# Performance work log

Hardware: AMD Instinct MI355X
Metric: run time of the kernel (lower is better)

Reference implementation:

```python
import jax, jax.numpy as jnp
import numpy as np

N_LAYERS = 4
NEG_SLOPE = 0.2  # GATv2 leaky_relu slope


def _segment_softmax(alpha, seg, num):
    # alpha: [E, H], seg: [E] target-node ids; every node has a self loop so no empty segments
    amax = jax.ops.segment_max(alpha, seg, num_segments=num)
    a = jnp.exp(alpha - amax[seg])
    denom = jax.ops.segment_sum(a, seg, num_segments=num)
    return a / denom[seg]


def _gat_block(x, relations, src, dst, rel_idx, Wl, bl, Wr, br, We, att, bias, Wb, bb):
    N, D = x.shape
    H = att.shape[0]
    C = att.shape[1]

    edge_attr = relations[rel_idx]  # [E, D]
    # add_self_loops with fill_value='mean': self-loop edge_attr = mean of incoming edge attrs
    deg = jax.ops.segment_sum(jnp.ones_like(dst, dtype=x.dtype), dst, num_segments=N)
    loop_attr = jax.ops.segment_sum(edge_attr, dst, num_segments=N) / jnp.maximum(deg, 1.0)[:, None]
    loops = jnp.arange(N, dtype=src.dtype)
    src_all = jnp.concatenate([src, loops])
    dst_all = jnp.concatenate([dst, loops])
    ea = jnp.concatenate([edge_attr, loop_attr], axis=0)  # [E+N, D]

    xl = (x @ Wl + bl).reshape(N, H, C)  # lin_l -> source transform
    xr = (x @ Wr + br).reshape(N, H, C)  # lin_r -> target transform
    eproj = (ea @ We).reshape(-1, H, C)  # lin_edge (no bias in PyG GATv2Conv)

    m = xl[src_all] + xr[dst_all] + eproj          # [E+N, H, C]
    m = jnp.where(m > 0, m, NEG_SLOPE * m)          # leaky_relu
    alpha = jnp.einsum('ehc,hc->eh', m, att)        # [E+N, H]
    alpha = _segment_softmax(alpha, dst_all, N)

    msg = xl[src_all] * alpha[..., None]            # [E+N, H, C]
    out = jax.ops.segment_sum(msg, dst_all, num_segments=N)  # [N, H, C]
    x_out = out.mean(axis=1) + bias                 # concat=False -> head mean, then bias

    # relation update: gnn.lin_edge -> relu -> block lin_edge
    r = jax.nn.relu(relations @ We)                 # [R, H*C]
    r_out = r @ Wb + bb                             # [R, D]
    return x_out, r_out


def setup_inputs() -> dict:
    key = jax.random.key(0)
    N, E, R, D, H = 10000, 40000, 2000, 128, 8
    L = N_LAYERS
    ks = jax.random.split(key, 16)
    s = 1.0 / np.sqrt(D)
    sb = 1.0 / np.sqrt(H * D)
    return {
        'x': jax.random.normal(ks[0], (N, D), dtype=jnp.float32),
        'edge_index': jax.random.randint(ks[1], (2, E), 0, N),
        'relations': jax.random.normal(ks[2], (R, D), dtype=jnp.float32),
        'relation_index': jax.random.randint(ks[3], (E,), 0, R),
        'Wl': jax.random.normal(ks[4], (L, D, H * D), dtype=jnp.float32) * s,
        'bl': jnp.zeros((L, H * D), dtype=jnp.float32),
        'Wr': jax.random.normal(ks[5], (L, D, H * D), dtype=jnp.float32) * s,
        'br': jnp.zeros((L, H * D), dtype=jnp.float32),
        'We': jax.random.normal(ks[6], (L, D, H * D), dtype=jnp.float32) * s,
        'att': jax.random.normal(ks[7], (L, H, D), dtype=jnp.float32) * s,
        'bias': jnp.zeros((L, D), dtype=jnp.float32),
        'Wb': jax.random.normal(ks[8], (L, H * D, D), dtype=jnp.float32) * sb,
        'bb': jnp.zeros((L, D), dtype=jnp.float32),
    }


def reference(x, edge_index, relations, relation_index, Wl, bl, Wr, br, We, att, bias, Wb, bb):
    src, dst = edge_index[0], edge_index[1]
    for l in range(N_LAYERS):
        x, relations = _gat_block(x, relations, src, dst, relation_index,
                                  Wl[l], bl[l], Wr[l], br[l], We[l], att[l],
                                  bias[l], Wb[l], bb[l])
    return (x, relations)
```

## Files before the change

kernel.cpp:

```cpp
#include <hip/hip_runtime.h>
#include <hip/hip_bf16.h>
#include <math.h>

#define NEG_SLOPE 0.2f
#define N_LAYERS 4

typedef __bf16 bf16_t;
typedef __attribute__((ext_vector_type(8))) __bf16 bf16x8;
typedef __attribute__((ext_vector_type(4))) __bf16 bf16x4;
typedef __attribute__((ext_vector_type(4))) float f32x4;
typedef __attribute__((ext_vector_type(8))) float f32x8;

static __device__ __forceinline__ float leaky(float v){ return v > 0.f ? v : NEG_SLOPE * v; }

static __device__ __forceinline__ bf16x8 relu8(bf16x8 v){
#pragma unroll
  for(int i = 0; i < 8; ++i) v[i] = (v[i] > (bf16_t)0.f) ? v[i] : (bf16_t)0.f;
  return v;
}


__global__ void fill_int_kernel(int* __restrict__ p, int v, int n){
  int i = blockIdx.x*blockDim.x + threadIdx.x;
  if(i < n) p[i] = v;
}

__global__ void hist_kernel(const int* __restrict__ dst, int E, int* __restrict__ deg){
  int e = blockIdx.x*blockDim.x + threadIdx.x;
  if(e < E) atomicAdd(&deg[dst[e]], 1);
}

__global__ void scan_kernel(const int* __restrict__ deg, int* __restrict__ offs, int N){
  __shared__ int wsum[4];
  int t = threadIdx.x, lane = t & 63, w = t >> 6;
  int carry = 0;
  for(int base = 0; base < N; base += 256){
    int v = (base + t < N) ? deg[base + t] : 0;
    int s = v;
#pragma unroll
    for(int o = 1; o < 64; o <<= 1){
      int u = __shfl_up(s, o);
      if(lane >= o) s += u;
    }
    if(lane == 63) wsum[w] = s;
    __syncthreads();
    int woff = 0;
    for(int i = 0; i < w; ++i) woff += wsum[i];
    if(base + t < N) offs[base + t + 1] = carry + woff + s;
    int tot = wsum[0] + wsum[1] + wsum[2] + wsum[3];
    __syncthreads();
    carry += tot;
  }
  if(t == 0) offs[0] = 0;
}

__global__ void scatter_kernel(const int* __restrict__ src, const int* __restrict__ dst,
                               const int* __restrict__ rel, int E,
                               const int* __restrict__ offs, int* __restrict__ cursor,
                               int* __restrict__ srcs, int* __restrict__ rels){
  int e = blockIdx.x*blockDim.x + threadIdx.x;
  if(e < E){
    int d = dst[e];
    int pos = offs[d] + atomicAdd(&cursor[d], 1);
    srcs[pos] = src[e];
    rels[pos] = rel[e];
  }
}


__global__ void deg_bhist_kernel(const int* __restrict__ offs, int N, int* __restrict__ blkhist){
  __shared__ int h[256];
  int t = threadIdx.x;
  h[t] = 0; __syncthreads();
  int i = blockIdx.x * 256 + t;
  if(i < N){
    int d = offs[i+1] - offs[i]; if(d > 255) d = 255;
    atomicAdd(&h[d], 1);
  }
  __syncthreads();
  blkhist[blockIdx.x * 256 + t] = h[t];
}

__global__ void deg_base_kernel(int* __restrict__ blkhist, int nb){
  __shared__ int tot[256];
  int d = threadIdx.x;
  int s = 0;
  for(int b = 0; b < nb; ++b){
    int v = blkhist[b * 256 + d];
    blkhist[b * 256 + d] = s;
    s += v;
  }
  tot[d] = s; __syncthreads();
  int start = 0;
  for(int k = d + 1; k < 256; ++k) start += tot[k];
  for(int b = 0; b < nb; ++b) blkhist[b * 256 + d] += start;
}

__global__ void deg_place_kernel(const int* __restrict__ offs, int N,
                                 const int* __restrict__ blkhist, int* __restrict__ order){
  __shared__ int cur[256];
  int t = threadIdx.x;
  cur[t] = blkhist[blockIdx.x * 256 + t];
  __syncthreads();
  int i = blockIdx.x * 256 + t;
  if(i < N){
    int d = offs[i+1] - offs[i]; if(d > 255) d = 255;
    int pos = atomicAdd(&cur[d], 1);
    order[pos] = i;
  }
}


__global__ void transpose_split_all_kernel(
    const float* __restrict__ Wl, const float* __restrict__ Wr,
    const float* __restrict__ We, const float* __restrict__ Wb,
    bf16_t* __restrict__ tWlh, bf16_t* __restrict__ tWll,
    bf16_t* __restrict__ tWrh, bf16_t* __restrict__ tWrl,
    bf16_t* __restrict__ tWeh, bf16_t* __restrict__ tWel,
    bf16_t* __restrict__ tWbh, bf16_t* __restrict__ tWbl){
  __shared__ float t[32][33];
  const int z = blockIdx.z, type = z >> 2, layer = z & 3;
  const int K  = (type < 3) ? 128 : 1024;
  const int Nn = (type < 3) ? 1024 : 128;
  const float* W; bf16_t* Th; bf16_t* Tl;
  if(type == 0){ W = Wl; Th = tWlh; Tl = tWll; }
  else if(type == 1){ W = Wr; Th = tWrh; Tl = tWrl; }
  else if(type == 2){ W = We; Th = tWeh; Tl = tWel; }
  else { W = Wb; Th = tWbh; Tl = tWbl; }
  size_t wo = (size_t)layer * 131072;
  W += wo; Th += wo; Tl += wo;
  const int nbx = K / 32;
  const int bx = blockIdx.x % nbx, by = blockIdx.x / nbx;
  const int k0 = bx * 32, n0 = by * 32;
  const int tx = threadIdx.x, ty = threadIdx.y;
#pragma unroll
  for(int i = 0; i < 4; ++i)
    t[ty*4 + i][tx] = W[(size_t)(k0 + ty*4 + i) * Nn + n0 + tx];
  __syncthreads();
#pragma unroll
  for(int i = 0; i < 4; ++i){
    int n = ty*4 + i;
    float v = t[tx][n];
    bf16_t h = (bf16_t)v;
    bf16_t l = (bf16_t)(v - (float)h);
    Th[(size_t)(n0 + n) * K + k0 + tx] = h;
    Tl[(size_t)(n0 + n) * K + k0 + tx] = l;
  }
}


__global__ __launch_bounds__(256, 3) void gemm_proj_kernel(
    const float* __restrict__ Ar, const float* __restrict__ Ax,
    const bf16_t* __restrict__ Axb,
    const bf16_t* __restrict__ Weh, const bf16_t* __restrict__ Wel,
    const bf16_t* __restrict__ Wlh, const bf16_t* __restrict__ Wll,
    const bf16_t* __restrict__ Wrh, const bf16_t* __restrict__ Wrl,
    const float* __restrict__ biasL, const float* __restrict__ biasR,
    const float* __restrict__ biasB, float* __restrict__ ro,
    bf16_t* __restrict__ rpb, bf16_t* __restrict__ xlb, bf16_t* __restrict__ xrb,
    int R, int Nn, int rjobs, int xjobs, int bjobs){
  constexpr int LDK = 40;
  __shared__ char smem[34816];
  bf16_t* Ah = (bf16_t*)smem;
  bf16_t* Bh = (bf16_t*)(smem + 10240);
  bf16_t* Bl = (bf16_t*)(smem + 20480);

  const int tid  = threadIdx.x;
  const int lane = tid & 63;
  const int wid  = tid >> 6;
  const int wm = wid >> 1, wn = wid & 1;
  const int l15 = lane & 15;
  const int kb  = (lane >> 4) * 8;

  int nwg = gridDim.x;
  int lin = blockIdx.x;
  int w = ((nwg & 7) == 0) ? ((lin & 7) * (nwg >> 3) + (lin >> 3)) : lin;
  int job, jw;
  if(w < rjobs){ job = 0; jw = w; }
  else if(w < rjobs + xjobs){ job = 1; jw = w - rjobs; }
  else if(w < rjobs + 2 * xjobs){ job = 2; jw = w - rjobs - xjobs; }
  else { job = 3; jw = w - rjobs - 2 * xjobs; }

  if(job == 3){
    int idx8 = (jw * 256 + tid) * 8;
    if(idx8 < R * 128){
      const float* bp = biasB + (idx8 & 127);
      *(float4*)(ro + idx8)     = *(const float4*)bp;
      *(float4*)(ro + idx8 + 4) = *(const float4*)(bp + 4);
    }
    return;
  }

  const float*  A   = (job == 0) ? Ar : Ax;
  const bf16_t* Bth = (job == 0) ? Weh : (job == 1) ? Wlh : Wrh;
  const bf16_t* Btl = (job == 0) ? Wel : (job == 1) ? Wll : Wrl;
  const int M = (job == 0) ? R : Nn;
  const int row0 = (jw >> 3) * 128, col0 = (jw & 7) * 128;
  const bool abf = (job != 0) && (Axb != nullptr);

  f32x4 acc[4][4];
#pragma unroll
  for(int m = 0; m < 4; ++m)
#pragma unroll
    for(int n = 0; n < 4; ++n) acc[m][n] = (f32x4){0.f, 0.f, 0.f, 0.f};

  for(int k0 = 0; k0 < 128; k0 += 32){
    __syncthreads();
    if(abf){
#pragma unroll
      for(int i = 0; i < 2; ++i){
        int f = tid + i * 256;
        int r = f >> 2, kq = f & 3;
        bf16x8 v = {};
        if(row0 + r < M) v = *(const bf16x8*)(Axb + (size_t)(row0 + r) * 128 + k0 + kq * 8);
        *(bf16x8*)&Ah[r * LDK + kq * 8] = v;
      }
    } else {
#pragma unroll
      for(int i = 0; i < 4; ++i){
        int f = tid + i * 256;
        int r = f >> 3, kq = f & 7;
        float4 v = make_float4(0.f, 0.f, 0.f, 0.f);
        if(row0 + r < M) v = *(const float4*)(A + (size_t)(row0 + r) * 128 + k0 + kq * 4);
        bf16x4 hv = (bf16x4){(bf16_t)v.x, (bf16_t)v.y, (bf16_t)v.z, (bf16_t)v.w};
        *(bf16x4*)&Ah[r * LDK + kq * 4] = hv;
      }
    }
#pragma unroll
    for(int i = 0; i < 2; ++i){
      int f = tid + i * 256;
      int n = f >> 2, kq = f & 3;
      size_t g = (size_t)(col0 + n) * 128 + k0 + kq * 8;
      *(bf16x8*)&Bh[n * LDK + kq * 8] = *(const bf16x8*)(Bth + g);
      *(bf16x8*)&Bl[n * LDK + kq * 8] = *(const bf16x8*)(Btl + g);
    }
    __syncthreads();

    bf16x8 ah[4], bh[4], bl[4];
#pragma unroll
    for(int m = 0; m < 4; ++m){
      int r = wm * 64 + m * 16 + l15;
      ah[m] = *(bf16x8*)&Ah[r * LDK + kb];
    }
#pragma unroll
    for(int n = 0; n < 4; ++n){
      int c = wn * 64 + n * 16 + l15;
      bh[n] = *(bf16x8*)&Bh[c * LDK + kb];
      bl[n] = *(bf16x8*)&Bl[c * LDK + kb];
    }
#pragma unroll
    for(int m = 0; m < 4; ++m)
#pragma unroll
      for(int n = 0; n < 4; ++n){
        acc[m][n] = __builtin_amdgcn_mfma_f32_16x16x32_bf16(ah[m], bh[n], acc[m][n], 0, 0, 0);
        acc[m][n] = __builtin_amdgcn_mfma_f32_16x16x32_bf16(ah[m], bl[n], acc[m][n], 0, 0, 0);
      }
  }

  const float* biasP = (job == 0) ? nullptr : (job == 1) ? biasL : biasR;
  bf16_t* dst = (job == 0) ? rpb : (job == 1) ? xlb : xrb;
  bf16_t* tile = (bf16_t*)smem;
  __syncthreads();
#pragma unroll
  for(int n = 0; n < 4; ++n){
    int col = wn * 64 + n * 16 + l15;
    float bv = biasP ? biasP[col0 + col] : 0.f;
#pragma unroll
    for(int m = 0; m < 4; ++m){
      int rb = wm * 64 + m * 16 + (lane >> 4) * 4;
#pragma unroll
      for(int r = 0; r < 4; ++r)
        tile[(rb + r) * 136 + col] = (bf16_t)(acc[m][n][r] + bv);
    }
  }
  __syncthreads();
#pragma unroll
  for(int i = 0; i < 8; ++i){
    int ei = i * 2048 + tid * 8;
    int rr = ei >> 7, cc = ei & 127;
    if(row0 + rr < M)
      *(bf16x8*)(dst + (size_t)(row0 + rr) * 1024 + col0 + cc) = *(bf16x8*)&tile[rr * 136 + cc];
  }
}


__global__ __launch_bounds__(256) void gemm_rel_kernel(
    const bf16_t* __restrict__ Ag,
    const bf16_t* __restrict__ Bth, const bf16_t* __restrict__ Btl,
    float* __restrict__ C, int M){
  constexpr int LDK = 40;
  __shared__ bf16_t Ah[128 * LDK];
  __shared__ bf16_t Bh[128 * LDK];
  __shared__ bf16_t Bl[128 * LDK];

  const int tid  = threadIdx.x;
  const int lane = tid & 63;
  const int wid  = tid >> 6;
  const int wm = wid >> 1, wn = wid & 1;
  const int row0 = blockIdx.y * 128;
  const int l15 = lane & 15;
  const int kb  = (lane >> 4) * 8;
  const int kbeg = blockIdx.z * 64;

  f32x4 acc[4][4];
#pragma unroll
  for(int m = 0; m < 4; ++m)
#pragma unroll
    for(int n = 0; n < 4; ++n) acc[m][n] = (f32x4){0.f, 0.f, 0.f, 0.f};

#pragma unroll
  for(int tt = 0; tt < 2; ++tt){
    int k0 = kbeg + tt * 32;
    __syncthreads();
#pragma unroll
    for(int i = 0; i < 2; ++i){
      int f = tid + i * 256;
      int r = f >> 2, kq = f & 3;
      bf16x8 vh = {};
      if(row0 + r < M)
        vh = relu8(*(const bf16x8*)(Ag + (size_t)(row0 + r) * 1024 + k0 + kq * 8));
      *(bf16x8*)&Ah[r * LDK + kq * 8] = vh;
      size_t gb = (size_t)r * 1024 + k0 + kq * 8;
      *(bf16x8*)&Bh[r * LDK + kq * 8] = *(const bf16x8*)(Bth + gb);
      *(bf16x8*)&Bl[r * LDK + kq * 8] = *(const bf16x8*)(Btl + gb);
    }
    __syncthreads();

    bf16x8 ah[4], bh[4], bl[4];
#pragma unroll
    for(int m = 0; m < 4; ++m){
      int r = wm * 64 + m * 16 + l15;
      ah[m] = *(bf16x8*)&Ah[r * LDK + kb];
    }
#pragma unroll
    for(int n = 0; n < 4; ++n){
      int c = wn * 64 + n * 16 + l15;
      bh[n] = *(bf16x8*)&Bh[c * LDK + kb];
      bl[n] = *(bf16x8*)&Bl[c * LDK + kb];
    }
#pragma unroll
    for(int m = 0; m < 4; ++m)
#pragma unroll
      for(int n = 0; n < 4; ++n){
        acc[m][n] = __builtin_amdgcn_mfma_f32_16x16x32_bf16(ah[m], bh[n], acc[m][n], 0, 0, 0);
        acc[m][n] = __builtin_amdgcn_mfma_f32_16x16x32_bf16(ah[m], bl[n], acc[m][n], 0, 0, 0);
      }
  }

#pragma unroll
  for(int n = 0; n < 4; ++n){
    int col = wn * 64 + n * 16 + l15;
    if(col < 128){
#pragma unroll
      for(int m = 0; m < 4; ++m){
        int rbase = row0 + wm * 64 + m * 16 + (lane >> 4) * 4;
#pragma unroll
        for(int r = 0; r < 4; ++r){
          if(rbase + r < M)
            atomicAdd(&C[(size_t)(rbase + r) * 128 + col], acc[m][n][r]);
        }
      }
    }
  }
}


__global__ __launch_bounds__(256) void node_fused_kernel(
    const bf16_t* __restrict__ xlb, const bf16_t* __restrict__ xrb,
    const bf16_t* __restrict__ rpb,
    const int* __restrict__ offs, const int* __restrict__ srcs, const int* __restrict__ rels,
    const int* __restrict__ order,
    const float* __restrict__ att, const float* __restrict__ bias,
    float* __restrict__ xout, bf16_t* __restrict__ xq, int N){
  __shared__ float tsh[2][128];
  const int wid  = threadIdx.x >> 6;
  const int lane = threadIdx.x & 63;
  const int nib  = wid >> 1;
  const int half = wid & 1;
  const int slot = blockIdx.x * 2 + nib;
  const bool active = slot < N;
  const int node = active ? order[slot] : 0;
  int beg = 0, end = 0;
  if(active){ beg = offs[node]; end = offs[node + 1]; }
  const float inv = 1.0f / fmaxf((float)(end - beg), 1.0f);

  const int o  = (half * 64 + lane) * 8;
  const int c0 = (lane & 15) * 8;
  const int h  = half * 4 + (lane >> 4);
  f32x8 av = *(const f32x8*)(att + h * 128 + c0);
  bf16x8 xrv = *(const bf16x8*)(xrb + (size_t)node * 1024 + o);
  f32x8 xr;
#pragma unroll
  for(int i = 0; i < 8; ++i) xr[i] = (float)xrv[i];

  f32x8 lac, num;
#pragma unroll
  for(int i = 0; i < 8; ++i){ lac[i] = 0.f; num[i] = 0.f; }
  float m = -INFINITY, den = 0.f;

  for(int p = beg; p < end; p += 4){
    int rem = end - p;
    int i1 = (rem > 1) ? p + 1 : p;
    int i2 = (rem > 2) ? p + 2 : p;
    int i3 = (rem > 3) ? p + 3 : p;
    float k1 = (rem > 1) ? 1.f : 0.f;
    float k2 = (rem > 2) ? 1.f : 0.f;
    float k3 = (rem > 3) ? 1.f : 0.f;
    int s0 = srcs[p],  r0 = rels[p];
    int s1 = srcs[i1], r1 = rels[i1];
    int s2 = srcs[i2], r2 = rels[i2];
    int s3 = srcs[i3], r3 = rels[i3];
    bf16x8 a0 = *(const bf16x8*)(xlb + (size_t)s0 * 1024 + o);
    bf16x8 b0 = *(const bf16x8*)(rpb + (size_t)r0 * 1024 + o);
    bf16x8 a1 = *(const bf16x8*)(xlb + (size_t)s1 * 1024 + o);
    bf16x8 b1 = *(const bf16x8*)(rpb + (size_t)r1 * 1024 + o);
    bf16x8 a2 = *(const bf16x8*)(xlb + (size_t)s2 * 1024 + o);
    bf16x8 b2 = *(const bf16x8*)(rpb + (size_t)r2 * 1024 + o);
    bf16x8 a3 = *(const bf16x8*)(xlb + (size_t)s3 * 1024 + o);
    bf16x8 b3 = *(const bf16x8*)(rpb + (size_t)r3 * 1024 + o);
    float l0 = 0.f, l1 = 0.f, l2 = 0.f, l3 = 0.f;
#pragma unroll
    for(int i = 0; i < 8; ++i){
      float v0 = (float)b0[i], v1 = (float)b1[i], v2 = (float)b2[i], v3 = (float)b3[i];
      lac[i] += v0 + k1 * v1 + k2 * v2 + k3 * v3;
      l0 += leaky((float)a0[i] + xr[i] + v0) * av[i];
      l1 += leaky((float)a1[i] + xr[i] + v1) * av[i];
      l2 += leaky((float)a2[i] + xr[i] + v2) * av[i];
      l3 += leaky((float)a3[i] + xr[i] + v3) * av[i];
    }
#pragma unroll
    for(int q = 8; q >= 1; q >>= 1){
      l0 += __shfl_xor(l0, q); l1 += __shfl_xor(l1, q);
      l2 += __shfl_xor(l2, q); l3 += __shfl_xor(l3, q);
    }
    l1 = (k1 > 0.f) ? l1 : -INFINITY;
    l2 = (k2 > 0.f) ? l2 : -INFINITY;
    l3 = (k3 > 0.f) ? l3 : -INFINITY;
    float nm = fmaxf(m, fmaxf(fmaxf(l0, l1), fmaxf(l2, l3)));
    float sc = __expf(m - nm);
    float w0 = __expf(l0 - nm), w1 = __expf(l1 - nm);
    float w2 = __expf(l2 - nm), w3 = __expf(l3 - nm);
    den = den * sc + w0 + w1 + w2 + w3;
#pragma unroll
    for(int i = 0; i < 8; ++i)
      num[i] = num[i] * sc + w0 * (float)a0[i] + w1 * (float)a1[i]
                           + w2 * (float)a2[i] + w3 * (float)a3[i];
    m = nm;
  }

  bf16x8 xlv = *(const bf16x8*)(xlb + (size_t)node * 1024 + o);
  float sl = 0.f;
#pragma unroll
  for(int i = 0; i < 8; ++i)
    sl += leaky((float)xlv[i] + xr[i] + lac[i] * inv) * av[i];
#pragma unroll
  for(int q = 8; q >= 1; q >>= 1) sl += __shfl_xor(sl, q);
  {
    float nm = fmaxf(m, sl);
    float sc = __expf(m - nm), wv = __expf(sl - nm);
    den = den * sc + wv;
#pragma unroll
    for(int i = 0; i < 8; ++i) num[i] = num[i] * sc + wv * (float)xlv[i];
    m = nm;
  }

  f32x8 t;
  float d = 1.0f / den;
#pragma unroll
  for(int i = 0; i < 8; ++i) t[i] = num[i] * d;
#pragma unroll
  for(int i = 0; i < 8; ++i) t[i] += __shfl_xor(t[i], 16);
#pragma unroll
  for(int i = 0; i < 8; ++i) t[i] += __shfl_xor(t[i], 32);

  if(half == 1 && lane < 16){
#pragma unroll
    for(int i = 0; i < 8; ++i) tsh[nib][lane * 8 + i] = t[i];
  }
  __syncthreads();
  if(active && half == 0 && lane < 16){
    const float* bp = bias + lane * 8;
    float q[8];
#pragma unroll
    for(int i = 0; i < 8; ++i) q[i] = (t[i] + tsh[nib][lane * 8 + i]) * 0.125f + bp[i];
    bf16x8 qb;
#pragma unroll
    for(int i = 0; i < 8; ++i) qb[i] = (bf16_t)q[i];
    *(bf16x8*)(xq + (size_t)node * 128 + lane * 8) = qb;
    if(xout){
      float* op = xout + (size_t)node * 128 + lane * 8;
      *(float4*)op       = make_float4(q[0], q[1], q[2], q[3]);
      *(float4*)(op + 4) = make_float4(q[4], q[5], q[6], q[7]);
    }
  }
}


extern "C" void kernel_launch(void* const* d_in, const int* in_sizes, int n_in,
                              void* d_out, int out_size, void* d_ws, size_t ws_size,
                              hipStream_t stream){
  const float* x0   = (const float*)d_in[0];
  const int*   ei   = (const int*)d_in[1];
  const float* rel0 = (const float*)d_in[2];
  const int*   ridx = (const int*)d_in[3];
  const float* Wl   = (const float*)d_in[4];
  const float* bl   = (const float*)d_in[5];
  const float* Wr   = (const float*)d_in[6];
  const float* br   = (const float*)d_in[7];
  const float* We   = (const float*)d_in[8];
  const float* att  = (const float*)d_in[9];
  const float* bias = (const float*)d_in[10];
  const float* Wb   = (const float*)d_in[11];
  const float* bb   = (const float*)d_in[12];

  const int D = 128, HC = 1024;
  const int N = in_sizes[0] / D;
  const int E = in_sizes[1] / 2;
  const int R = in_sizes[2] / D;
  const int WSZ = D * HC;
  const int NB = (N + 255) / 256;

  const int* src = ei;
  const int* dst = ei + E;

  char* ws = (char*)d_ws;
  size_t off = 0;
  auto alloc = [&](size_t bytes) -> void* {
    void* p = ws + off;
    off += (bytes + 255) & ~(size_t)255;
    return p;
  };
  bf16_t* xlb    = (bf16_t*)alloc((size_t)N * HC * 2);
  bf16_t* xrb    = (bf16_t*)alloc((size_t)N * HC * 2);
  bf16_t* rpb    = (bf16_t*)alloc((size_t)R * HC * 2);
  bf16_t* xqA    = (bf16_t*)alloc((size_t)N * D * 2);
  bf16_t* xqB    = (bf16_t*)alloc((size_t)N * D * 2);
  float*  rbufA  = (float*)alloc((size_t)R * D * 4);
  float*  rbufB  = (float*)alloc((size_t)R * D * 4);
  int* zbase   = (int*)alloc((size_t)(2 * N) * 4);
  int* deg     = zbase;
  int* cursor  = zbase + N;
  int* offs    = (int*)alloc((size_t)(N + 1) * 4);
  int* blkhist = (int*)alloc((size_t)NB * 256 * 4);
  int* order   = (int*)alloc((size_t)N * 4);
  int* srcs    = (int*)alloc((size_t)E * 4);
  int* rels    = (int*)alloc((size_t)E * 4);
  bf16_t* tWl_h = (bf16_t*)alloc((size_t)N_LAYERS * WSZ * 2);
  bf16_t* tWl_l = (bf16_t*)alloc((size_t)N_LAYERS * WSZ * 2);
  bf16_t* tWr_h = (bf16_t*)alloc((size_t)N_LAYERS * WSZ * 2);
  bf16_t* tWr_l = (bf16_t*)alloc((size_t)N_LAYERS * WSZ * 2);
  bf16_t* tWe_h = (bf16_t*)alloc((size_t)N_LAYERS * WSZ * 2);
  bf16_t* tWe_l = (bf16_t*)alloc((size_t)N_LAYERS * WSZ * 2);
  bf16_t* tWb_h = (bf16_t*)alloc((size_t)N_LAYERS * WSZ * 2);
  bf16_t* tWb_l = (bf16_t*)alloc((size_t)N_LAYERS * WSZ * 2);
  bf16_t* xq[2] = {xqA, xqB};
  float* rbuf[2] = {rbufA, rbufB};

  float* out_x = (float*)d_out;
  float* out_r = (float*)d_out + (size_t)N * D;

  fill_int_kernel<<<(2 * N + 255) / 256, 256, 0, stream>>>(zbase, 0, 2 * N);
  hist_kernel<<<(E + 255) / 256, 256, 0, stream>>>(dst, E, deg);
  scan_kernel<<<1, 256, 0, stream>>>(deg, offs, N);
  scatter_kernel<<<(E + 255) / 256, 256, 0, stream>>>(src, dst, ridx, E, offs, cursor, srcs, rels);
  deg_bhist_kernel<<<NB, 256, 0, stream>>>(offs, N, blkhist);
  deg_base_kernel<<<1, 256, 0, stream>>>(blkhist, NB);
  deg_place_kernel<<<NB, 256, 0, stream>>>(offs, N, blkhist, order);

  transpose_split_all_kernel<<<dim3(128, 1, 16), dim3(32, 8), 0, stream>>>(
      Wl, Wr, We, Wb, tWl_h, tWl_l, tWr_h, tWr_l, tWe_h, tWe_l, tWb_h, tWb_l);

  const int rjobs = ((R + 127) / 128) * (HC / 128);
  const int xjobs = ((N + 127) / 128) * (HC / 128);
  const int bjobs = 128;
  const int nwg = rjobs + 2 * xjobs + bjobs;

  for(int l = 0; l < N_LAYERS; ++l){
    const bf16_t* xq_in = (l == 0) ? nullptr : xq[(l + 1) & 1];
    bf16_t*       xq_out = xq[l & 1];
    float*        xo  = (l == N_LAYERS - 1) ? out_x : nullptr;
    const float*  rin = (l == 0) ? rel0 : rbuf[(l + 1) & 1];
    float*        ro  = (l == N_LAYERS - 1) ? out_r : rbuf[l & 1];
    size_t wo = (size_t)l * WSZ;
    const float* bl_l  = bl + (size_t)l * HC;
    const float* br_l  = br + (size_t)l * HC;
    const float* att_l = att + (size_t)l * 8 * 128;
    const float* bias_l= bias + (size_t)l * D;
    const float* bb_l  = bb + (size_t)l * D;

    gemm_proj_kernel<<<nwg, 256, 0, stream>>>(
        rin, x0, xq_in, tWe_h + wo, tWe_l + wo, tWl_h + wo, tWl_l + wo, tWr_h + wo, tWr_l + wo,
        bl_l, br_l, bb_l, ro, rpb, xlb, xrb, R, N, rjobs, xjobs, bjobs);
    node_fused_kernel<<<(2 * N + 3) / 4, 256, 0, stream>>>(
        xlb, xrb, rpb, offs, srcs, rels, order, att_l, bias_l, xo, xq_out, N);
    gemm_rel_kernel<<<dim3(1, (R + 127) / 128, 16), 256, 0, stream>>>(
        rpb, tWb_h + wo, tWb_l + wo, ro, R);
  }
}
```

Baseline: 395.0 us.

## Merge scatter and degree histogram launches, preload A tile, prefetch edge indices

Three separate changes. The scatter and per-block degree-histogram kernels become one launch whose blocks branch on blockIdx, saving a kernel launch. The projection GEMM now loads the full 128-wide A tile into shared memory once and streams only the B hi/lo slices per k-step, which raises shared memory use and may lower occupancy. The attention aggregation loop software-prefetches the next group of four source/relation indices so the dependent gathers wait less on index loads.

```diff
diff --git a/kernel.cpp b/kernel.cpp
--- a/kernel.cpp
+++ b/kernel.cpp
@@ -54,31 +54,32 @@
   if(t == 0) offs[0] = 0;
 }
 
-__global__ void scatter_kernel(const int* __restrict__ src, const int* __restrict__ dst,
-                               const int* __restrict__ rel, int E,
-                               const int* __restrict__ offs, int* __restrict__ cursor,
-                               int* __restrict__ srcs, int* __restrict__ rels){
-  int e = blockIdx.x*blockDim.x + threadIdx.x;
-  if(e < E){
-    int d = dst[e];
-    int pos = offs[d] + atomicAdd(&cursor[d], 1);
-    srcs[pos] = src[e];
-    rels[pos] = rel[e];
-  }
-}
-
-
-__global__ void deg_bhist_kernel(const int* __restrict__ offs, int N, int* __restrict__ blkhist){
+__global__ void scatter_bhist_kernel(const int* __restrict__ src, const int* __restrict__ dst,
+                                     const int* __restrict__ rel, int E,
+                                     const int* __restrict__ offs, int* __restrict__ cursor,
+                                     int* __restrict__ srcs, int* __restrict__ rels,
+                                     int N, int* __restrict__ blkhist, int SCB){
   __shared__ int h[256];
-  int t = threadIdx.x;
-  h[t] = 0; __syncthreads();
-  int i = blockIdx.x * 256 + t;
-  if(i < N){
-    int d = offs[i+1] - offs[i]; if(d > 255) d = 255;
-    atomicAdd(&h[d], 1);
-  }
-  __syncthreads();
-  blkhist[blockIdx.x * 256 + t] = h[t];
+  if((int)blockIdx.x < SCB){
+    int e = blockIdx.x * 256 + threadIdx.x;
+    if(e < E){
+      int d = dst[e];
+      int pos = offs[d] + atomicAdd(&cursor[d], 1);
+      srcs[pos] = src[e];
+      rels[pos] = rel[e];
+    }
+  } else {
+    int b = blockIdx.x - SCB;
+    int t = threadIdx.x;
+    h[t] = 0; __syncthreads();
+    int i = b * 256 + t;
+    if(i < N){
+      int d = offs[i+1] - offs[i]; if(d > 255) d = 255;
+      atomicAdd(&h[d], 1);
+    }
+    __syncthreads();
+    blkhist[b * 256 + t] = h[t];
+  }
 }
 
 __global__ void deg_base_kernel(int* __restrict__ blkhist, int nb){
@@ -159,11 +160,11 @@
     const float* __restrict__ biasB, float* __restrict__ ro,
     bf16_t* __restrict__ rpb, bf16_t* __restrict__ xlb, bf16_t* __restrict__ xrb,
     int R, int Nn, int rjobs, int xjobs, int bjobs){
-  constexpr int LDK = 40;
-  __shared__ char smem[34816];
-  bf16_t* Ah = (bf16_t*)smem;
-  bf16_t* Bh = (bf16_t*)(smem + 10240);
-  bf16_t* Bl = (bf16_t*)(smem + 20480);
+  constexpr int LDA  = 136;
+  constexpr int LDBB = 72;
+  __shared__ char smem[53248];
+  bf16_t* Ah  = (bf16_t*)smem;
+  bf16_t* Bhl = (bf16_t*)(smem + 34816);
 
   const int tid  = threadIdx.x;
   const int lane = tid & 63;
@@ -198,55 +199,56 @@
   const int row0 = (jw >> 3) * 128, col0 = (jw & 7) * 128;
   const bool abf = (job != 0) && (Axb != nullptr);
 
+  if(abf){
+#pragma unroll
+    for(int i = 0; i < 8; ++i){
+      int f = tid + i * 256;
+      int r = f >> 4, kq = f & 15;
+      bf16x8 v = {};
+      if(row0 + r < M) v = *(const bf16x8*)(Axb + (size_t)(row0 + r) * 128 + kq * 8);
+      *(bf16x8*)&Ah[r * LDA + kq * 8] = v;
+    }
+  } else {
+#pragma unroll
+    for(int i = 0; i < 16; ++i){
+      int f = tid + i * 256;
+      int r = f >> 5, kq = f & 31;
+      float4 v = make_float4(0.f, 0.f, 0.f, 0.f);
+      if(row0 + r < M) v = *(const float4*)(A + (size_t)(row0 + r) * 128 + kq * 4);
+      bf16x4 hv = (bf16x4){(bf16_t)v.x, (bf16_t)v.y, (bf16_t)v.z, (bf16_t)v.w};
+      *(bf16x4*)&Ah[r * LDA + kq * 4] = hv;
+    }
+  }
+#pragma unroll
+  for(int i = 0; i < 2; ++i){
+    int f = tid + i * 256;
+    int n = f >> 2, kq = f & 3;
+    size_t g = (size_t)(col0 + n) * 128 + kq * 8;
+    *(bf16x8*)&Bhl[n * LDBB + kq * 8]      = *(const bf16x8*)(Bth + g);
+    *(bf16x8*)&Bhl[n * LDBB + 32 + kq * 8] = *(const bf16x8*)(Btl + g);
+  }
+  __syncthreads();
+
   f32x4 acc[4][4];
 #pragma unroll
   for(int m = 0; m < 4; ++m)
 #pragma unroll
     for(int n = 0; n < 4; ++n) acc[m][n] = (f32x4){0.f, 0.f, 0.f, 0.f};
 
-  for(int k0 = 0; k0 < 128; k0 += 32){
-    __syncthreads();
-    if(abf){
-#pragma unroll
-      for(int i = 0; i < 2; ++i){
-        int f = tid + i * 256;
-        int r = f >> 2, kq = f & 3;
-        bf16x8 v = {};
-        if(row0 + r < M) v = *(const bf16x8*)(Axb + (size_t)(row0 + r) * 128 + k0 + kq * 8);
-        *(bf16x8*)&Ah[r * LDK + kq * 8] = v;
-      }
-    } else {
-#pragma unroll
-      for(int i = 0; i < 4; ++i){
-        int f = tid + i * 256;
-        int r = f >> 3, kq = f & 7;
-        float4 v = make_float4(0.f, 0.f, 0.f, 0.f);
-        if(row0 + r < M) v = *(const float4*)(A + (size_t)(row0 + r) * 128 + k0 + kq * 4);
-        bf16x4 hv = (bf16x4){(bf16_t)v.x, (bf16_t)v.y, (bf16_t)v.z, (bf16_t)v.w};
-        *(bf16x4*)&Ah[r * LDK + kq * 4] = hv;
-      }
-    }
-#pragma unroll
-    for(int i = 0; i < 2; ++i){
-      int f = tid + i * 256;
-      int n = f >> 2, kq = f & 3;
-      size_t g = (size_t)(col0 + n) * 128 + k0 + kq * 8;
-      *(bf16x8*)&Bh[n * LDK + kq * 8] = *(const bf16x8*)(Bth + g);
-      *(bf16x8*)&Bl[n * LDK + kq * 8] = *(const bf16x8*)(Btl + g);
-    }
-    __syncthreads();
-
+#pragma unroll
+  for(int step = 0; step < 4; ++step){
+    const int k0 = step * 32;
     bf16x8 ah[4], bh[4], bl[4];
 #pragma unroll
     for(int m = 0; m < 4; ++m){
       int r = wm * 64 + m * 16 + l15;
-      ah[m] = *(bf16x8*)&Ah[r * LDK + kb];
+      ah[m] = *(bf16x8*)&Ah[r * LDA + k0 + kb];
     }
 #pragma unroll
     for(int n = 0; n < 4; ++n){
       int c = wn * 64 + n * 16 + l15;
-      bh[n] = *(bf16x8*)&Bh[c * LDK + kb];
-      bl[n] = *(bf16x8*)&Bl[c * LDK + kb];
+      bh[n] = *(bf16x8*)&Bhl[c * LDBB + kb];
+      bl[n] = *(bf16x8*)&Bhl[c * LDBB + 32 + kb];
     }
 #pragma unroll
     for(int m = 0; m < 4; ++m)
@@ -255,11 +257,23 @@
         acc[m][n] = __builtin_amdgcn_mfma_f32_16x16x32_bf16(ah[m], bh[n], acc[m][n], 0, 0, 0);
         acc[m][n] = __builtin_amdgcn_mfma_f32_16x16x32_bf16(ah[m], bl[n], acc[m][n], 0, 0, 0);
       }
+    if(step < 3){
+      __syncthreads();
+#pragma unroll
+      for(int i = 0; i < 2; ++i){
+        int f = tid + i * 256;
+        int n = f >> 2, kq = f & 3;
+        size_t g = (size_t)(col0 + n) * 128 + k0 + 32 + kq * 8;
+        *(bf16x8*)&Bhl[n * LDBB + kq * 8]      = *(const bf16x8*)(Bth + g);
+        *(bf16x8*)&Bhl[n * LDBB + 32 + kq * 8] = *(const bf16x8*)(Btl + g);
+      }
+      __syncthreads();
+    }
   }
 
   const float* biasP = (job == 0) ? nullptr : (job == 1) ? biasL : biasR;
   bf16_t* dst = (job == 0) ? rpb : (job == 1) ? xlb : xrb;
-  bf16_t* tile = (bf16_t*)smem;
+  bf16_t* tile = Ah;
   __syncthreads();
 #pragma unroll
   for(int n = 0; n < 4; ++n){
@@ -398,26 +412,50 @@
   for(int i = 0; i < 8; ++i){ lac[i] = 0.f; num[i] = 0.f; }
   float m = -INFINITY, den = 0.f;
 
-  for(int p = beg; p < end; p += 4){
+  int p = beg;
+  int cs0 = 0, cs1 = 0, cs2 = 0, cs3 = 0, cr0 = 0, cr1 = 0, cr2 = 0, cr3 = 0;
+  float k1 = 0.f, k2 = 0.f, k3 = 0.f;
+  if(p < end){
     int rem = end - p;
     int i1 = (rem > 1) ? p + 1 : p;
     int i2 = (rem > 2) ? p + 2 : p;
     int i3 = (rem > 3) ? p + 3 : p;
-    float k1 = (rem > 1) ? 1.f : 0.f;
-    float k2 = (rem > 2) ? 1.f : 0.f;
-    float k3 = (rem > 3) ? 1.f : 0.f;
-    int s0 = srcs[p],  r0 = rels[p];
-    int s1 = srcs[i1], r1 = rels[i1];
-    int s2 = srcs[i2], r2 = rels[i2];
-    int s3 = srcs[i3], r3 = rels[i3];
-    bf16x8 a0 = *(const bf16x8*)(xlb + (size_t)s0 * 1024 + o);
-    bf16x8 b0 = *(const bf16x8*)(rpb + (size_t)r0 * 1024 + o);
-    bf16x8 a1 = *(const bf16x8*)(xlb + (size_t)s1 * 1024 + o);
-    bf16x8 b1 = *(const bf16x8*)(rpb + (size_t)r1 * 1024 + o);
-    bf16x8 a2 = *(const bf16x8*)(xlb + (size_t)s2 * 1024 + o);
-    bf16x8 b2 = *(const bf16x8*)(rpb + (size_t)r2 * 1024 + o);
-    bf16x8 a3 = *(const bf16x8*)(xlb + (size_t)s3 * 1024 + o);
-    bf16x8 b3 = *(const bf16x8*)(rpb + (size_t)r3 * 1024 + o);
+    k1 = (rem > 1) ? 1.f : 0.f;
+    k2 = (rem > 2) ? 1.f : 0.f;
+    k3 = (rem > 3) ? 1.f : 0.f;
+    cs0 = srcs[p];  cr0 = rels[p];
+    cs1 = srcs[i1]; cr1 = rels[i1];
+    cs2 = srcs[i2]; cr2 = rels[i2];
+    cs3 = srcs[i3]; cr3 = rels[i3];
+  }
+
+  while(p < end){
+    bf16x8 a0 = *(const bf16x8*)(xlb + (size_t)cs0 * 1024 + o);
+    bf16x8 b0 = *(const bf16x8*)(rpb + (size_t)cr0 * 1024 + o);
+    bf16x8 a1 = *(const bf16x8*)(xlb + (size_t)cs1 * 1024 + o);
+    bf16x8 b1 = *(const bf16x8*)(rpb + (size_t)cr1 * 1024 + o);
+    bf16x8 a2 = *(const bf16x8*)(xlb + (size_t)cs2 * 1024 + o);
+    bf16x8 b2 = *(const bf16x8*)(rpb + (size_t)cr2 * 1024 + o);
+    bf16x8 a3 = *(const bf16x8*)(xlb + (size_t)cs3 * 1024 + o);
+    bf16x8 b3 = *(const bf16x8*)(rpb + (size_t)cr3 * 1024 + o);
+
+    int np = p + 4;
+    int ns0 = 0, ns1 = 0, ns2 = 0, ns3 = 0, nr0 = 0, nr1 = 0, nr2 = 0, nr3 = 0;
+    float nk1 = 0.f, nk2 = 0.f, nk3 = 0.f;
+    if(np < end){
+      int rem = end - np;
+      int i1 = (rem > 1) ? np + 1 : np;
+      int i2 = (rem > 2) ? np + 2 : np;
+      int i3 = (rem > 3) ? np + 3 : np;
+      nk1 = (rem > 1) ? 1.f : 0.f;
+      nk2 = (rem > 2) ? 1.f : 0.f;
+      nk3 = (rem > 3) ? 1.f : 0.f;
+      ns0 = srcs[np]; nr0 = rels[np];
+      ns1 = srcs[i1]; nr1 = rels[i1];
+      ns2 = srcs[i2]; nr2 = rels[i2];
+      ns3 = srcs[i3]; nr3 = rels[i3];
+    }
+
     float l0 = 0.f, l1 = 0.f, l2 = 0.f, l3 = 0.f;
 #pragma unroll
     for(int i = 0; i < 8; ++i){
@@ -446,6 +484,11 @@
       num[i] = num[i] * sc + w0 * (float)a0[i] + w1 * (float)a1[i]
                            + w2 * (float)a2[i] + w3 * (float)a3[i];
     m = nm;
+
+    p = np;
+    cs0 = ns0; cs1 = ns1; cs2 = ns2; cs3 = ns3;
+    cr0 = nr0; cr1 = nr1; cr2 = nr2; cr3 = nr3;
+    k1 = nk1; k2 = nk2; k3 = nk3;
   }
 
   bf16x8 xlv = *(const bf16x8*)(xlb + (size_t)node * 1024 + o);
@@ -519,6 +562,7 @@
   const int R = in_sizes[2] / D;
   const int WSZ = D * HC;
   const int NB = (N + 255) / 256;
+  const int SCB = (E + 255) / 256;
 
   const int* src = ei;
   const int* dst = ei + E;
@@ -562,8 +606,8 @@
   fill_int_kernel<<<(2 * N + 255) / 256, 256, 0, stream>>>(zbase, 0, 2 * N);
   hist_kernel<<<(E + 255) / 256, 256, 0, stream>>>(dst, E, deg);
   scan_kernel<<<1, 256, 0, stream>>>(deg, offs, N);
-  scatter_kernel<<<(E + 255) / 256, 256, 0, stream>>>(src, dst, ridx, E, offs, cursor, srcs, rels);
-  deg_bhist_kernel<<<NB, 256, 0, stream>>>(offs, N, blkhist);
+  scatter_bhist_kernel<<<SCB + NB, 256, 0, stream>>>(
+      src, dst, ridx, E, offs, cursor, srcs, rels, N, blkhist, SCB);
   deg_base_kernel<<<1, 256, 0, stream>>>(blkhist, NB);
   deg_place_kernel<<<NB, 256, 0, stream>>>(offs, N, blkhist, order);
 
```

New measurement: 386.7 us. -2.1%, faster.
